# Kernel tuning notes

Hardware: AMD Instinct MI355X
Metric: run time of the kernel (lower is better)

## Reference

```python
import jax, jax.numpy as jnp
import numpy as np

NUM_HEADS = 16
HEIGHT = 32
WIDTH = 32
FEATURES_DIM = HEIGHT * WIDTH  # 1024
EMBED_DIM = 1024


def setup_inputs() -> dict:
    key = jax.random.key(0)
    ks = jax.random.split(key, 9)
    s_in = 1.0 / np.sqrt(FEATURES_DIM)
    s_e = 1.0 / np.sqrt(EMBED_DIM)
    return {
        "x": jax.random.normal(ks[0], (16, 512, HEIGHT, WIDTH), dtype=jnp.float32),
        "Wq": jax.random.uniform(ks[1], (EMBED_DIM, FEATURES_DIM), jnp.float32, -s_in, s_in),
        "bq": jax.random.uniform(ks[2], (EMBED_DIM,), jnp.float32, -s_in, s_in),
        "Wk": jax.random.uniform(ks[3], (EMBED_DIM, FEATURES_DIM), jnp.float32, -s_in, s_in),
        "bk": jax.random.uniform(ks[4], (EMBED_DIM,), jnp.float32, -s_in, s_in),
        "Wv": jax.random.uniform(ks[5], (EMBED_DIM, FEATURES_DIM), jnp.float32, -s_in, s_in),
        "bv": jax.random.uniform(ks[6], (EMBED_DIM,), jnp.float32, -s_in, s_in),
        "Wo": jax.random.uniform(ks[7], (FEATURES_DIM, EMBED_DIM), jnp.float32, -s_e, s_e),
        "bo": jax.random.uniform(ks[8], (FEATURES_DIM,), jnp.float32, -s_e, s_e),
    }


def reference(x, Wq, bq, Wk, bk, Wv, bv, Wo, bo):
    B, C, H, W = x.shape
    nh = NUM_HEADS
    hd = EMBED_DIM // nh
    xf = x.reshape(B, C, H * W)  # [B, C, F] - channel tokens
    q = xf @ Wq.T + bq  # [B, C, E]
    k = xf @ Wk.T + bk
    v = xf @ Wv.T + bv
    q = q.reshape(B, C, nh, hd).transpose(0, 2, 1, 3)  # [B, nh, C, hd]
    k = k.reshape(B, C, nh, hd).transpose(0, 2, 1, 3)
    v = v.reshape(B, C, nh, hd).transpose(0, 2, 1, 3)
    scores = jnp.einsum("bhcd,bhkd->bhck", q, k) / jnp.sqrt(jnp.float32(hd))
    attn = jax.nn.softmax(scores, axis=-1)
    out = jnp.einsum("bhck,bhkd->bhcd", attn, v)  # [B, nh, C, hd]
    out = out.transpose(0, 2, 1, 3).reshape(B, C, EMBED_DIM)
    out = out @ Wo.T + bo  # [B, C, F]
    return out.reshape(B, C, H, W)
```

## Files before the change

kernel.cpp:

```cpp
#include <hip/hip_runtime.h>


typedef unsigned short u16;
typedef __attribute__((ext_vector_type(8))) short short8;
typedef __attribute__((ext_vector_type(4))) float f32x4;
typedef __attribute__((ext_vector_type(4))) unsigned short u16x4;

#define MFMA16(a, b, c) __builtin_amdgcn_mfma_f32_16x16x32_bf16(a, b, c, 0, 0, 0)

__device__ __forceinline__ u16 f2bf(float x) {
  unsigned u = __float_as_uint(x);
  u += 0x7FFFu + ((u >> 16) & 1u);
  return (u16)(u >> 16);
}

__device__ __forceinline__ void async16(const void* g, void* l) {
  __builtin_amdgcn_global_load_lds(
      (__attribute__((address_space(1))) unsigned int*)(g),
      (__attribute__((address_space(3))) unsigned int*)(l), 16, 0, 0);
}

__global__ __launch_bounds__(256) void cvt_bf16(const float* __restrict__ s,
                                                u16* __restrict__ d, int n4) {
  int i = blockIdx.x * 256 + threadIdx.x;
  if (i >= n4) return;
  f32x4 v = ((const f32x4*)s)[i];
  u16x4 o;
#pragma unroll
  for (int j = 0; j < 4; ++j) o[j] = f2bf(v[j]);
  ((u16x4*)d)[i] = o;
}

__device__ __forceinline__ void gemm8(const u16* __restrict__ A,
                                      const u16* __restrict__ W,
                                      int m0, int n0, u16* lds,
                                      f32x4 acc[4][4]) {
  const int t = threadIdx.x;
  const int wave = t >> 6, lane = t & 63, lr = lane & 15, lg = lane >> 4;
  const int wr = wave >> 2, wn = wave & 3;
  const int srow = t >> 3;
  const int scol = ((t & 7) ^ ((t >> 3) & 7)) << 3;
  const u16* gA = A + (size_t)(m0 + srow) * 1024 + scol;
  const u16* gB = W + (size_t)(n0 + srow) * 1024 + scol;
  u16* stA = lds + wave * 512;
  u16* stB = lds + 8192 + wave * 512;
  const int aoff = (wr * 64 + lr) * 64;
  const int boff = (wn * 64 + lr) * 64;
  const int sw0 = (lg ^ (lr & 7)) << 3;
  const int sw1 = ((4 ^ lg) ^ (lr & 7)) << 3;

#define STAGEA(buf, k0)                                   \
  {                                                       \
    async16(gA + (k0), stA + (buf) * 24576);              \
    async16(gA + 65536 + (k0), stA + (buf) * 24576 + 4096); \
  }
#define STAGEB2(buf, k0, j)                                             \
  {                                                                     \
    async16(gB + (j) * 65536 + (k0), stB + (buf) * 24576 + (j) * 4096); \
    async16(gB + ((j) + 1) * 65536 + (k0),                              \
            stB + (buf) * 24576 + ((j) + 1) * 4096);                    \
  }

  STAGEA(0, 0); STAGEB2(0, 0, 0); STAGEB2(0, 0, 2);
  STAGEA(1, 64); STAGEB2(1, 64, 0); STAGEB2(1, 64, 2);
  asm volatile("s_waitcnt vmcnt(6)" ::: "memory");
  __builtin_amdgcn_s_barrier();

#pragma unroll
  for (int tt = 0; tt < 16; ++tt) {
    const int cb = tt % 3, nb = (tt + 2) % 3;
    const bool st = (tt < 14);
    const int kn = (tt + 2) * 64;
    const u16* la = lds + cb * 24576 + aoff;
    const u16* lb = lds + cb * 24576 + 8192 + boff;
    short8 av[4], b0, b1;
#pragma unroll
    for (int m = 0; m < 4; ++m) av[m] = *(const short8*)(la + m * 1024 + sw0);
    b0 = *(const short8*)(lb + 0 * 1024 + sw0);
    b1 = *(const short8*)(lb + 1 * 1024 + sw0);
    if (st) STAGEA(nb, kn);
    __builtin_amdgcn_s_barrier();
    __builtin_amdgcn_s_setprio(1);
#pragma unroll
    for (int m = 0; m < 4; ++m) {
      acc[m][0] = MFMA16(av[m], b0, acc[m][0]);
      acc[m][1] = MFMA16(av[m], b1, acc[m][1]);
    }
    __builtin_amdgcn_s_setprio(0);
    __builtin_amdgcn_s_barrier();
    b0 = *(const short8*)(lb + 2 * 1024 + sw0);
    b1 = *(const short8*)(lb + 3 * 1024 + sw0);
    if (st) STAGEB2(nb, kn, 0);
    __builtin_amdgcn_s_barrier();
    __builtin_amdgcn_s_setprio(1);
#pragma unroll
    for (int m = 0; m < 4; ++m) {
      acc[m][2] = MFMA16(av[m], b0, acc[m][2]);
      acc[m][3] = MFMA16(av[m], b1, acc[m][3]);
    }
    __builtin_amdgcn_s_setprio(0);
    __builtin_amdgcn_s_barrier();
#pragma unroll
    for (int m = 0; m < 4; ++m) av[m] = *(const short8*)(la + m * 1024 + sw1);
    b0 = *(const short8*)(lb + 0 * 1024 + sw1);
    b1 = *(const short8*)(lb + 1 * 1024 + sw1);
    if (st) STAGEB2(nb, kn, 2);
    __builtin_amdgcn_s_barrier();
    __builtin_amdgcn_s_setprio(1);
#pragma unroll
    for (int m = 0; m < 4; ++m) {
      acc[m][0] = MFMA16(av[m], b0, acc[m][0]);
      acc[m][1] = MFMA16(av[m], b1, acc[m][1]);
    }
    __builtin_amdgcn_s_setprio(0);
    __builtin_amdgcn_s_barrier();
    b0 = *(const short8*)(lb + 2 * 1024 + sw1);
    b1 = *(const short8*)(lb + 3 * 1024 + sw1);
    __builtin_amdgcn_s_barrier();
    __builtin_amdgcn_s_setprio(1);
#pragma unroll
    for (int m = 0; m < 4; ++m) {
      acc[m][2] = MFMA16(av[m], b0, acc[m][2]);
      acc[m][3] = MFMA16(av[m], b1, acc[m][3]);
    }
    __builtin_amdgcn_s_setprio(0);
    if (tt < 14) {
      asm volatile("s_waitcnt vmcnt(6)" ::: "memory");
    } else {
      asm volatile("s_waitcnt vmcnt(0)" ::: "memory");
    }
    __builtin_amdgcn_s_barrier();
  }
#undef STAGEA
#undef STAGEB2
}

__global__ __launch_bounds__(512, 1) void gemm_qkv(
    const u16* __restrict__ xb, const u16* __restrict__ wq,
    const u16* __restrict__ wk, const u16* __restrict__ wv,
    const float* __restrict__ bq, const float* __restrict__ bk,
    const float* __restrict__ bv, u16* __restrict__ qo, u16* __restrict__ ko,
    u16* __restrict__ vo) {
  __shared__ u16 lds[73728];
  const int id = blockIdx.x;
  const int lid = (id & 7) * 96 + (id >> 3);
  const int z = lid >> 8;
  const int rem = lid & 255;
  const int m0 = (rem >> 2) * 128, n0 = (rem & 3) * 256;
  const u16* W = (z == 0) ? wq : (z == 1) ? wk : wv;
  const float* bias = (z == 0) ? bq : (z == 1) ? bk : bv;
  u16* outp = (z == 0) ? qo : (z == 1) ? ko : vo;
  f32x4 acc[4][4];
#pragma unroll
  for (int i = 0; i < 4; ++i)
#pragma unroll
    for (int j = 0; j < 4; ++j) acc[i][j] = (f32x4){0.f, 0.f, 0.f, 0.f};
  gemm8(xb, W, m0, n0, lds, acc);

  const int t = threadIdx.x;
  const int wave = t >> 6, lane = t & 63, lr = lane & 15, lg = lane >> 4;
  const int wr = wave >> 2, wn = wave & 3;
  float bb[4];
#pragma unroll
  for (int nf = 0; nf < 4; ++nf) bb[nf] = bias[n0 + wn * 64 + nf * 16 + lr];
#pragma unroll
  for (int mf = 0; mf < 4; ++mf)
#pragma unroll
    for (int nf = 0; nf < 4; ++nf)
#pragma unroll
      for (int r = 0; r < 4; ++r) {
        int m = m0 + wr * 64 + mf * 16 + lg * 4 + r;
        int n = n0 + wn * 64 + nf * 16 + lr;
        float val = acc[mf][nf][r] + bb[nf];
        int b_ = m >> 9, c = m & 511, h = n >> 6, dd = n & 63;
        int idx = (z == 2) ? ((((b_ << 4) + h) << 15) + (dd << 9) + c)
                           : ((((b_ << 4) + h) << 15) + (c << 6) + dd);
        outp[idx] = f2bf(val);
      }
}

__global__ __launch_bounds__(512, 1) void gemm_oproj(const u16* __restrict__ ab,
                                                     const u16* __restrict__ wo,
                                                     const float* __restrict__ bo,
                                                     float* __restrict__ out) {
  __shared__ u16 lds[73728];
  const int id = blockIdx.x;
  const int lid = (id & 7) * 32 + (id >> 3);
  const int m0 = (lid >> 2) * 128, n0 = (lid & 3) * 256;
  f32x4 acc[4][4];
#pragma unroll
  for (int i = 0; i < 4; ++i)
#pragma unroll
    for (int j = 0; j < 4; ++j) acc[i][j] = (f32x4){0.f, 0.f, 0.f, 0.f};
  gemm8(ab, wo, m0, n0, lds, acc);

  const int t = threadIdx.x;
  const int wave = t >> 6, lane = t & 63, lr = lane & 15, lg = lane >> 4;
  const int wr = wave >> 2, wn = wave & 3;
  float bb[4];
#pragma unroll
  for (int nf = 0; nf < 4; ++nf) bb[nf] = bo[n0 + wn * 64 + nf * 16 + lr];
#pragma unroll
  for (int mf = 0; mf < 4; ++mf)
#pragma unroll
    for (int nf = 0; nf < 4; ++nf)
#pragma unroll
      for (int r = 0; r < 4; ++r) {
        int m = m0 + wr * 64 + mf * 16 + lg * 4 + r;
        int n = n0 + wn * 64 + nf * 16 + lr;
        out[m * 1024 + n] = acc[mf][nf][r] + bb[nf];
      }
}

__global__ __launch_bounds__(512, 2) void attn_kernel(
    const u16* __restrict__ qb, const u16* __restrict__ kb,
    const u16* __restrict__ vb, u16* __restrict__ ab) {
  __shared__ u16 lK[32768];
  __shared__ u16 lV[32768];
  __shared__ u16 lP[8192];
  const int t = threadIdx.x;
  const int bh = blockIdx.x;
  const int b_ = bh >> 4, h_ = bh & 15;
  const u16* kg = kb + bh * 32768;
  const u16* vg = vb + bh * 32768;
#pragma unroll
  for (int i = 0; i < 8; ++i) {
    int row = i * 64 + (t >> 3), slot = t & 7;
    short8 kv = *(const short8*)(kg + row * 64 + slot * 8);
    *(short8*)(lK + row * 64 + ((slot ^ (row & 7)) << 3)) = kv;
    int vrow = i * 8 + (t >> 6), vslot = t & 63;
    short8 vv = *(const short8*)(vg + vrow * 512 + vslot * 8);
    *(short8*)(lV + vrow * 512 + ((vslot ^ (vrow & 7)) << 3)) = vv;
  }
  __syncthreads();

  const int wv_ = t >> 6, lane = t & 63, lr = lane & 15, lg = lane >> 4;
  u16* lPw = lP + wv_ * 1024;
  const u16* qg = qb + bh * 32768;
  const float sc = 0.125f * 1.44269504088896f;

#pragma unroll 1
  for (int qi = 0; qi < 4; ++qi) {
    const int qrow = (wv_ * 4 + qi) * 16;
    short8 a0 = *(const short8*)(qg + (qrow + lr) * 64 + lg * 8);
    short8 a1 = *(const short8*)(qg + (qrow + lr) * 64 + 32 + lg * 8);
    f32x4 s[32];
#pragma unroll
    for (int f = 0; f < 32; ++f) {
      const u16* kr = lK + (f * 16 + lr) * 64;
      short8 k0 = *(const short8*)(kr + ((lg ^ (lr & 7)) << 3));
      short8 k1 = *(const short8*)(kr + (((4 + lg) ^ (lr & 7)) << 3));
      f32x4 z4 = (f32x4){0.f, 0.f, 0.f, 0.f};
      z4 = MFMA16(a0, k0, z4);
      z4 = MFMA16(a1, k1, z4);
      s[f] = z4;
    }
    float inv[4];
#pragma unroll
    for (int r = 0; r < 4; ++r) {
      float m_ = s[0][r];
#pragma unroll
      for (int f = 1; f < 32; ++f) m_ = fmaxf(m_, s[f][r]);
      m_ = fmaxf(m_, __shfl_xor(m_, 1));
      m_ = fmaxf(m_, __shfl_xor(m_, 2));
      m_ = fmaxf(m_, __shfl_xor(m_, 4));
      m_ = fmaxf(m_, __shfl_xor(m_, 8));
      float sm = 0.f;
#pragma unroll
      for (int f = 0; f < 32; ++f) {
        float e = exp2f((s[f][r] - m_) * sc);
        s[f][r] = e;
        sm += e;
      }
      sm += __shfl_xor(sm, 1);
      sm += __shfl_xor(sm, 2);
      sm += __shfl_xor(sm, 4);
      sm += __shfl_xor(sm, 8);
      inv[r] = 1.f / sm;
    }
    f32x4 o[4];
#pragma unroll
    for (int i = 0; i < 4; ++i) o[i] = (f32x4){0.f, 0.f, 0.f, 0.f};
#pragma unroll
    for (int ch = 0; ch < 8; ++ch) {
#pragma unroll
      for (int cf = 0; cf < 4; ++cf)
#pragma unroll
        for (int r = 0; r < 4; ++r) {
          int q = lg * 4 + r, kc = cf * 16 + lr;
          lPw[q * 64 + (((kc >> 3) ^ (q & 7)) << 3) + (kc & 7)] =
              f2bf(s[ch * 4 + cf][r]);
        }
      asm volatile("s_waitcnt lgkmcnt(0)" ::: "memory");
      const u16* pr = lPw + lr * 64;
      short8 pa0 = *(const short8*)(pr + ((lg ^ (lr & 7)) << 3));
      short8 pa1 = *(const short8*)(pr + (((4 + lg) ^ (lr & 7)) << 3));
#pragma unroll
      for (int df = 0; df < 4; ++df) {
        const u16* vr = lV + (df * 16 + lr) * 512;
        short8 v0 = *(const short8*)(vr + (((ch * 8 + lg) ^ (lr & 7)) << 3));
        short8 v1 =
            *(const short8*)(vr + (((ch * 8 + 4 + lg) ^ (lr & 7)) << 3));
        o[df] = MFMA16(pa0, v0, o[df]);
        o[df] = MFMA16(pa1, v1, o[df]);
      }
    }
#pragma unroll
    for (int df = 0; df < 4; ++df)
#pragma unroll
      for (int r = 0; r < 4; ++r) {
        int q = qrow + lg * 4 + r, dd = df * 16 + lr;
        ab[(b_ * 512 + q) * 1024 + h_ * 64 + dd] = f2bf(o[df][r] * inv[r]);
      }
  }
}

extern "C" void kernel_launch(void* const* d_in, const int* in_sizes, int n_in,
                              void* d_out, int out_size, void* d_ws,
                              size_t ws_size, hipStream_t stream) {
  (void)in_sizes; (void)n_in; (void)out_size;
  const float* x  = (const float*)d_in[0];
  const float* Wq = (const float*)d_in[1];
  const float* bq = (const float*)d_in[2];
  const float* Wk = (const float*)d_in[3];
  const float* bk = (const float*)d_in[4];
  const float* Wv = (const float*)d_in[5];
  const float* bv = (const float*)d_in[6];
  const float* Wo = (const float*)d_in[7];
  const float* bo = (const float*)d_in[8];
  float* out = (float*)d_out;

  if (ws_size < 75497472u) return;
  u16* xb  = (u16*)d_ws;
  u16* wqb = xb + 8388608;
  u16* wkb = wqb + 1048576;
  u16* wvb = wkb + 1048576;
  u16* wob = wvb + 1048576;
  u16* qbuf = wob + 1048576;
  u16* kbuf = qbuf + 8388608;
  u16* vbuf = kbuf + 8388608;
  u16* abuf = xb;

  cvt_bf16<<<8192, 256, 0, stream>>>(x, xb, 2097152);
  cvt_bf16<<<1024, 256, 0, stream>>>(Wq, wqb, 262144);
  cvt_bf16<<<1024, 256, 0, stream>>>(Wk, wkb, 262144);
  cvt_bf16<<<1024, 256, 0, stream>>>(Wv, wvb, 262144);
  cvt_bf16<<<1024, 256, 0, stream>>>(Wo, wob, 262144);

  gemm_qkv<<<768, 512, 0, stream>>>(xb, wqb, wkb, wvb, bq, bk, bv,
                                    qbuf, kbuf, vbuf);
  attn_kernel<<<256, 512, 0, stream>>>(qbuf, kbuf, vbuf, abuf);
  gemm_oproj<<<256, 512, 0, stream>>>(abuf, wob, bo, out);
}
```

Before: 174.3 us.

## Switch GEMMs to 32x32 MFMA, drop inner barriers, merge bf16 conversion launches

Rewrites the shared GEMM core to use 32x32x16 bf16 MFMA tiles (2x2 per wave) instead of 16x16x32 tiles. All LDS fragments for a K-step are loaded up front and the multiple intra-iteration barriers are removed, leaving one barrier per stage. Launch bounds are raised to allow two blocks per CU. The five fp32-to-bf16 conversion launches are merged into a single kernel that writes the contiguous workspace. Two blocks per CU needs 2x144KB of LDS, which exceeds the 160KB per CU on this hardware, so occupancy likely stays at one block per CU.

```diff
diff --git a/kernel.cpp b/kernel.cpp
--- a/kernel.cpp
+++ b/kernel.cpp
@@ -4,9 +4,11 @@
 typedef unsigned short u16;
 typedef __attribute__((ext_vector_type(8))) short short8;
 typedef __attribute__((ext_vector_type(4))) float f32x4;
+typedef __attribute__((ext_vector_type(16))) float f32x16;
 typedef __attribute__((ext_vector_type(4))) unsigned short u16x4;
 
 #define MFMA16(a, b, c) __builtin_amdgcn_mfma_f32_16x16x32_bf16(a, b, c, 0, 0, 0)
+#define MFMA32(a, b, c) __builtin_amdgcn_mfma_f32_32x32x16_bf16(a, b, c, 0, 0, 0)
 
 __device__ __forceinline__ u16 f2bf(float x) {
   unsigned u = __float_as_uint(x);
@@ -20,23 +22,34 @@
       (__attribute__((address_space(3))) unsigned int*)(l), 16, 0, 0);
 }
 
-__global__ __launch_bounds__(256) void cvt_bf16(const float* __restrict__ s,
-                                                u16* __restrict__ d, int n4) {
-  int i = blockIdx.x * 256 + threadIdx.x;
-  if (i >= n4) return;
-  f32x4 v = ((const f32x4*)s)[i];
+__global__ __launch_bounds__(256) void cvt_all(
+    const float* __restrict__ x, const float* __restrict__ wq,
+    const float* __restrict__ wk, const float* __restrict__ wv,
+    const float* __restrict__ wo, u16* __restrict__ dst) {
+  int g = blockIdx.x * 256 + threadIdx.x;
+  const float* s;
+  int off;
+  if (g < 2097152) {
+    s = x; off = g;
+  } else {
+    int r = g - 2097152;
+    int w = r >> 18;
+    off = r & 262143;
+    s = (w == 0) ? wq : (w == 1) ? wk : (w == 2) ? wv : wo;
+  }
+  f32x4 v = ((const f32x4*)s)[off];
   u16x4 o;
 #pragma unroll
   for (int j = 0; j < 4; ++j) o[j] = f2bf(v[j]);
-  ((u16x4*)d)[i] = o;
-}
-
-__device__ __forceinline__ void gemm8(const u16* __restrict__ A,
-                                      const u16* __restrict__ W,
-                                      int m0, int n0, u16* lds,
-                                      f32x4 acc[4][4]) {
+  ((u16x4*)dst)[g] = o;
+}
+
+__device__ __forceinline__ void gemm32(const u16* __restrict__ A,
+                                       const u16* __restrict__ W,
+                                       int m0, int n0, u16* lds,
+                                       f32x16 acc[2][2]) {
   const int t = threadIdx.x;
-  const int wave = t >> 6, lane = t & 63, lr = lane & 15, lg = lane >> 4;
+  const int wave = t >> 6, lane = t & 63, r31 = lane & 31, l5 = lane >> 5;
   const int wr = wave >> 2, wn = wave & 3;
   const int srow = t >> 3;
   const int scol = ((t & 7) ^ ((t >> 3) & 7)) << 3;
@@ -44,85 +57,54 @@
   const u16* gB = W + (size_t)(n0 + srow) * 1024 + scol;
   u16* stA = lds + wave * 512;
   u16* stB = lds + 8192 + wave * 512;
-  const int aoff = (wr * 64 + lr) * 64;
-  const int boff = (wn * 64 + lr) * 64;
-  const int sw0 = (lg ^ (lr & 7)) << 3;
-  const int sw1 = ((4 ^ lg) ^ (lr & 7)) << 3;
-
-#define STAGEA(buf, k0)                                   \
-  {                                                       \
-    async16(gA + (k0), stA + (buf) * 24576);              \
+  const int xk = r31 & 7;
+  const int arow = (wr * 64 + r31) * 64;
+  const int brow = 8192 + (wn * 64 + r31) * 64;
+  int soff[4];
+#pragma unroll
+  for (int ks = 0; ks < 4; ++ks) soff[ks] = ((ks * 2 + l5) ^ xk) << 3;
+
+#define STAGEA(buf, k0)                                     \
+  {                                                         \
+    async16(gA + (k0), stA + (buf) * 24576);                \
     async16(gA + 65536 + (k0), stA + (buf) * 24576 + 4096); \
   }
-#define STAGEB2(buf, k0, j)                                             \
-  {                                                                     \
-    async16(gB + (j) * 65536 + (k0), stB + (buf) * 24576 + (j) * 4096); \
-    async16(gB + ((j) + 1) * 65536 + (k0),                              \
-            stB + (buf) * 24576 + ((j) + 1) * 4096);                    \
-  }
-
-  STAGEA(0, 0); STAGEB2(0, 0, 0); STAGEB2(0, 0, 2);
-  STAGEA(1, 64); STAGEB2(1, 64, 0); STAGEB2(1, 64, 2);
+#define STAGEB(buf, k0)                                                   \
+  {                                                                       \
+    async16(gB + (k0), stB + (buf) * 24576);                              \
+    async16(gB + 65536 + (k0), stB + (buf) * 24576 + 4096);               \
+    async16(gB + 131072 + (k0), stB + (buf) * 24576 + 8192);              \
+    async16(gB + 196608 + (k0), stB + (buf) * 24576 + 12288);             \
+  }
+
+  STAGEA(0, 0); STAGEB(0, 0);
+  STAGEA(1, 64); STAGEB(1, 64);
   asm volatile("s_waitcnt vmcnt(6)" ::: "memory");
   __builtin_amdgcn_s_barrier();
 
 #pragma unroll
   for (int tt = 0; tt < 16; ++tt) {
-    const int cb = tt % 3, nb = (tt + 2) % 3;
-    const bool st = (tt < 14);
-    const int kn = (tt + 2) * 64;
-    const u16* la = lds + cb * 24576 + aoff;
-    const u16* lb = lds + cb * 24576 + 8192 + boff;
-    short8 av[4], b0, b1;
-#pragma unroll
-    for (int m = 0; m < 4; ++m) av[m] = *(const short8*)(la + m * 1024 + sw0);
-    b0 = *(const short8*)(lb + 0 * 1024 + sw0);
-    b1 = *(const short8*)(lb + 1 * 1024 + sw0);
-    if (st) STAGEA(nb, kn);
-    __builtin_amdgcn_s_barrier();
+    const u16* bufp = lds + (tt % 3) * 24576;
+    short8 av[2][4], bv[2][4];
+#pragma unroll
+    for (int ks = 0; ks < 4; ++ks) {
+      av[0][ks] = *(const short8*)(bufp + arow + soff[ks]);
+      av[1][ks] = *(const short8*)(bufp + arow + 2048 + soff[ks]);
+      bv[0][ks] = *(const short8*)(bufp + brow + soff[ks]);
+      bv[1][ks] = *(const short8*)(bufp + brow + 2048 + soff[ks]);
+    }
+    if (tt < 14) {
+      const int nb = (tt + 2) % 3, kn = (tt + 2) * 64;
+      STAGEA(nb, kn); STAGEB(nb, kn);
+    }
     __builtin_amdgcn_s_setprio(1);
 #pragma unroll
-    for (int m = 0; m < 4; ++m) {
-      acc[m][0] = MFMA16(av[m], b0, acc[m][0]);
-      acc[m][1] = MFMA16(av[m], b1, acc[m][1]);
-    }
-    __builtin_amdgcn_s_setprio(0);
-    __builtin_amdgcn_s_barrier();
-    b0 = *(const short8*)(lb + 2 * 1024 + sw0);
-    b1 = *(const short8*)(lb + 3 * 1024 + sw0);
-    if (st) STAGEB2(nb, kn, 0);
-    __builtin_amdgcn_s_barrier();
-    __builtin_amdgcn_s_setprio(1);
-#pragma unroll
-    for (int m = 0; m < 4; ++m) {
-      acc[m][2] = MFMA16(av[m], b0, acc[m][2]);
-      acc[m][3] = MFMA16(av[m], b1, acc[m][3]);
-    }
-    __builtin_amdgcn_s_setprio(0);
-    __builtin_amdgcn_s_barrier();
-#pragma unroll
-    for (int m = 0; m < 4; ++m) av[m] = *(const short8*)(la + m * 1024 + sw1);
-    b0 = *(const short8*)(lb + 0 * 1024 + sw1);
-    b1 = *(const short8*)(lb + 1 * 1024 + sw1);
-    if (st) STAGEB2(nb, kn, 2);
-    __builtin_amdgcn_s_barrier();
-    __builtin_amdgcn_s_setprio(1);
-#pragma unroll
-    for (int m = 0; m < 4; ++m) {
-      acc[m][0] = MFMA16(av[m], b0, acc[m][0]);
-      acc[m][1] = MFMA16(av[m], b1, acc[m][1]);
-    }
-    __builtin_amdgcn_s_setprio(0);
-    __builtin_amdgcn_s_barrier();
-    b0 = *(const short8*)(lb + 2 * 1024 + sw1);
-    b1 = *(const short8*)(lb + 3 * 1024 + sw1);
-    __builtin_amdgcn_s_barrier();
-    __builtin_amdgcn_s_setprio(1);
-#pragma unroll
-    for (int m = 0; m < 4; ++m) {
-      acc[m][2] = MFMA16(av[m], b0, acc[m][2]);
-      acc[m][3] = MFMA16(av[m], b1, acc[m][3]);
-    }
+    for (int ks = 0; ks < 4; ++ks)
+#pragma unroll
+      for (int mf = 0; mf < 2; ++mf)
+#pragma unroll
+        for (int nf = 0; nf < 2; ++nf)
+          acc[mf][nf] = MFMA32(av[mf][ks], bv[nf][ks], acc[mf][nf]);
     __builtin_amdgcn_s_setprio(0);
     if (tt < 14) {
       asm volatile("s_waitcnt vmcnt(6)" ::: "memory");
@@ -132,10 +114,10 @@
     __builtin_amdgcn_s_barrier();
   }
 #undef STAGEA
-#undef STAGEB2
-}
-
-__global__ __launch_bounds__(512, 1) void gemm_qkv(
+#undef STAGEB
+}
+
+__global__ __launch_bounds__(512, 2) void gemm_qkv(
     const u16* __restrict__ xb, const u16* __restrict__ wq,
     const u16* __restrict__ wk, const u16* __restrict__ wv,
     const float* __restrict__ bq, const float* __restrict__ bk,
@@ -150,27 +132,29 @@
   const u16* W = (z == 0) ? wq : (z == 1) ? wk : wv;
   const float* bias = (z == 0) ? bq : (z == 1) ? bk : bv;
   u16* outp = (z == 0) ? qo : (z == 1) ? ko : vo;
-  f32x4 acc[4][4];
-#pragma unroll
-  for (int i = 0; i < 4; ++i)
-#pragma unroll
-    for (int j = 0; j < 4; ++j) acc[i][j] = (f32x4){0.f, 0.f, 0.f, 0.f};
-  gemm8(xb, W, m0, n0, lds, acc);
+  f32x16 acc[2][2];
+#pragma unroll
+  for (int i = 0; i < 2; ++i)
+#pragma unroll
+    for (int j = 0; j < 2; ++j)
+#pragma unroll
+      for (int r = 0; r < 16; ++r) acc[i][j][r] = 0.f;
+  gemm32(xb, W, m0, n0, lds, acc);
 
   const int t = threadIdx.x;
-  const int wave = t >> 6, lane = t & 63, lr = lane & 15, lg = lane >> 4;
+  const int wave = t >> 6, lane = t & 63, r31 = lane & 31, l5 = lane >> 5;
   const int wr = wave >> 2, wn = wave & 3;
-  float bb[4];
-#pragma unroll
-  for (int nf = 0; nf < 4; ++nf) bb[nf] = bias[n0 + wn * 64 + nf * 16 + lr];
-#pragma unroll
-  for (int mf = 0; mf < 4; ++mf)
-#pragma unroll
-    for (int nf = 0; nf < 4; ++nf)
-#pragma unroll
-      for (int r = 0; r < 4; ++r) {
-        int m = m0 + wr * 64 + mf * 16 + lg * 4 + r;
-        int n = n0 + wn * 64 + nf * 16 + lr;
+  float bb[2];
+#pragma unroll
+  for (int nf = 0; nf < 2; ++nf) bb[nf] = bias[n0 + wn * 64 + nf * 32 + r31];
+#pragma unroll
+  for (int mf = 0; mf < 2; ++mf)
+#pragma unroll
+    for (int nf = 0; nf < 2; ++nf)
+#pragma unroll
+      for (int r = 0; r < 16; ++r) {
+        int m = m0 + wr * 64 + mf * 32 + (r & 3) + ((r >> 2) << 3) + (l5 << 2);
+        int n = n0 + wn * 64 + nf * 32 + r31;
         float val = acc[mf][nf][r] + bb[nf];
         int b_ = m >> 9, c = m & 511, h = n >> 6, dd = n & 63;
         int idx = (z == 2) ? ((((b_ << 4) + h) << 15) + (dd << 9) + c)
@@ -179,7 +163,7 @@
       }
 }
 
-__global__ __launch_bounds__(512, 1) void gemm_oproj(const u16* __restrict__ ab,
+__global__ __launch_bounds__(512, 2) void gemm_oproj(const u16* __restrict__ ab,
                                                      const u16* __restrict__ wo,
                                                      const float* __restrict__ bo,
                                                      float* __restrict__ out) {
@@ -187,27 +171,29 @@
   const int id = blockIdx.x;
   const int lid = (id & 7) * 32 + (id >> 3);
   const int m0 = (lid >> 2) * 128, n0 = (lid & 3) * 256;
-  f32x4 acc[4][4];
-#pragma unroll
-  for (int i = 0; i < 4; ++i)
-#pragma unroll
-    for (int j = 0; j < 4; ++j) acc[i][j] = (f32x4){0.f, 0.f, 0.f, 0.f};
-  gemm8(ab, wo, m0, n0, lds, acc);
+  f32x16 acc[2][2];
+#pragma unroll
+  for (int i = 0; i < 2; ++i)
+#pragma unroll
+    for (int j = 0; j < 2; ++j)
+#pragma unroll
+      for (int r = 0; r < 16; ++r) acc[i][j][r] = 0.f;
+  gemm32(ab, wo, m0, n0, lds, acc);
 
   const int t = threadIdx.x;
-  const int wave = t >> 6, lane = t & 63, lr = lane & 15, lg = lane >> 4;
+  const int wave = t >> 6, lane = t & 63, r31 = lane & 31, l5 = lane >> 5;
   const int wr = wave >> 2, wn = wave & 3;
-  float bb[4];
-#pragma unroll
-  for (int nf = 0; nf < 4; ++nf) bb[nf] = bo[n0 + wn * 64 + nf * 16 + lr];
-#pragma unroll
-  for (int mf = 0; mf < 4; ++mf)
-#pragma unroll
-    for (int nf = 0; nf < 4; ++nf)
-#pragma unroll
-      for (int r = 0; r < 4; ++r) {
-        int m = m0 + wr * 64 + mf * 16 + lg * 4 + r;
-        int n = n0 + wn * 64 + nf * 16 + lr;
+  float bb[2];
+#pragma unroll
+  for (int nf = 0; nf < 2; ++nf) bb[nf] = bo[n0 + wn * 64 + nf * 32 + r31];
+#pragma unroll
+  for (int mf = 0; mf < 2; ++mf)
+#pragma unroll
+    for (int nf = 0; nf < 2; ++nf)
+#pragma unroll
+      for (int r = 0; r < 16; ++r) {
+        int m = m0 + wr * 64 + mf * 32 + (r & 3) + ((r >> 2) << 3) + (l5 << 2);
+        int n = n0 + wn * 64 + nf * 32 + r31;
         out[m * 1024 + n] = acc[mf][nf][r] + bb[nf];
       }
 }
@@ -341,12 +327,7 @@
   u16* vbuf = kbuf + 8388608;
   u16* abuf = xb;
 
-  cvt_bf16<<<8192, 256, 0, stream>>>(x, xb, 2097152);
-  cvt_bf16<<<1024, 256, 0, stream>>>(Wq, wqb, 262144);
-  cvt_bf16<<<1024, 256, 0, stream>>>(Wk, wkb, 262144);
-  cvt_bf16<<<1024, 256, 0, stream>>>(Wv, wvb, 262144);
-  cvt_bf16<<<1024, 256, 0, stream>>>(Wo, wob, 262144);
-
+  cvt_all<<<12288, 256, 0, stream>>>(x, Wq, Wk, Wv, Wo, xb);
   gemm_qkv<<<768, 512, 0, stream>>>(xb, wqb, wkb, wvb, bq, bk, bv,
                                     qbuf, kbuf, vbuf);
   attn_kernel<<<256, 512, 0, stream>>>(qbuf, kbuf, vbuf, abuf);
```

After: 188.0 us. 1.08x slower.
